# Optimization experiments

Measured on AMD Instinct MI355X. Metric: run time of the kernel, lower is better.

## Reference

```python
import jax, jax.numpy as jnp
import numpy as np

HIDDEN = 1024
HEADS = 16
HEAD_DIM = HIDDEN // HEADS
MAX_SEQ = 2048
BATCH = 2
SEQ = 2048


def setup_inputs() -> dict:
    key = jax.random.key(0)
    ks = jax.random.split(key, 6)
    x = jax.random.normal(ks[0], (BATCH, SEQ, HIDDEN), dtype=jnp.float32)
    # torch Linear params expressed as [in, out] weight + bias
    W1 = jax.random.normal(ks[1], (HIDDEN, 4 * HIDDEN), dtype=jnp.float32) * (HIDDEN ** -0.5)
    b1 = jnp.zeros((4 * HIDDEN,), dtype=jnp.float32)
    W2 = jax.random.normal(ks[2], (HIDDEN, HIDDEN), dtype=jnp.float32) * (HIDDEN ** -0.5)
    b2 = jnp.zeros((HIDDEN,), dtype=jnp.float32)
    rel_table = jax.random.normal(ks[3], (2 * MAX_SEQ - 1, HEADS), dtype=jnp.float32) * 0.02
    # causal mask [B, S, S]; True = keep
    attn_mask = jnp.broadcast_to(jnp.tril(jnp.ones((SEQ, SEQ), dtype=bool)), (BATCH, SEQ, SEQ))
    return {"x": x, "W1": W1, "b1": b1, "W2": W2, "b2": b2,
            "rel_table": rel_table, "attn_mask": attn_mask}


def reference(x, W1, b1, W2, b2, rel_table, attn_mask):
    B, S, H = x.shape
    # fused projection + SiLU, then chunk into U, Q, K, V
    activated = jax.nn.silu(jnp.einsum('bsh,hf->bsf', x, W1) + b1)
    U, Qp, Kp, Vp = jnp.split(activated, 4, axis=-1)
    # [B, nH, S, hd]
    def heads(t):
        return t.reshape(B, S, HEADS, HEAD_DIM).transpose(0, 2, 1, 3)
    Q, K, V = heads(Qp), heads(Kp), heads(Vp)
    scale = HEAD_DIM ** -0.5
    scores = jnp.einsum('bnqd,bnkd->bnqk', Q, K) * scale
    # relative position bias gather: idx[i,j] = i - j + MAX_SEQ - 1
    pos = jnp.arange(S)
    rel_idx = pos[:, None] - pos[None, :] + (MAX_SEQ - 1)  # [S, S]
    rel_bias = rel_table[rel_idx].transpose(2, 0, 1)[None]  # [1, nH, S, S]
    scores = scores + rel_bias
    attn = jax.nn.silu(scores)
    attn = jnp.where(attn_mask[:, None, :, :], attn, 0.0)
    out = jnp.einsum('bnqk,bnkd->bnqd', attn, V)
    out = out.transpose(0, 2, 1, 3).reshape(B, S, H)
    gated = out * U
    return jnp.einsum('bsh,hf->bsf', gated, W2) + b2
```

## Files before the change

kernel.cpp:

```cpp
#include <hip/hip_runtime.h>
#include <hip/hip_bf16.h>
#include <math.h>

#define HIDDEN   1024
#define HEADS    16
#define HEAD_DIM 64
#define SEQ      2048
#define BATCH    2
#define FDIM     4096
#define MTOT     4096
#define MAXSEQ   2048

typedef __bf16 bf16x8 __attribute__((ext_vector_type(8)));
typedef float  f32x4  __attribute__((ext_vector_type(4)));
typedef unsigned short u16;

__device__ __forceinline__ float silu_fast(float v) {
    return v * __builtin_amdgcn_rcpf(1.f + __expf(-v));
}

__device__ __forceinline__ u16 f2bf(float f) {
    union { float f; unsigned u; } v; v.f = f;
    unsigned r = v.u + 0x7FFFu + ((v.u >> 16) & 1u);
    return (u16)(r >> 16);
}
__device__ __forceinline__ float bf2f(u16 b) {
    union { unsigned u; float f; } v; v.u = ((unsigned)b) << 16;
    return v.f;
}
__device__ __forceinline__ unsigned pk2(float a, float b) {
    union { __hip_bfloat162 h; unsigned u; } z;
    z.h = __float22bfloat162_rn(make_float2(a, b));
    return z.u;
}

__device__ __forceinline__ void gload16(const void* g, void* l) {
    __builtin_amdgcn_global_load_lds(
        (const __attribute__((address_space(1))) void*)g,
        (__attribute__((address_space(3))) void*)l, 16, 0, 0);
}

__global__ __launch_bounds__(256) void prep_kernel(
    const float* __restrict__ X, const float* __restrict__ W1,
    const float* __restrict__ W2,
    u16* __restrict__ Xb, u16* __restrict__ W1t, u16* __restrict__ W2t,
    unsigned* __restrict__ ticket)
{
    __shared__ u16 T[64][72];
    const int tid = threadIdx.x;
    const int bid = blockIdx.x;

    if (bid == 0 && tid == 0) *ticket = 0u;

    if (bid < 2048) {
        int idx = (bid * 256 + tid) * 8;
        float4 a = *(const float4*)&X[idx];
        float4 b = *(const float4*)&X[idx + 4];
        uint4 pk = make_uint4(pk2(a.x, a.y), pk2(a.z, a.w),
                              pk2(b.x, b.y), pk2(b.z, b.w));
        *(uint4*)&Xb[idx] = pk;
        return;
    }

    const float* W; u16* Wt; int rows, cols, r0, c0;
    if (bid < 3072) {
        int t = bid - 2048;
        W = W1; Wt = W1t; rows = HIDDEN; cols = FDIM;
        c0 = (t & 63) * 64; r0 = (t >> 6) * 64;
    } else {
        int t = bid - 3072;
        W = W2; Wt = W2t; rows = HIDDEN; cols = HIDDEN;
        c0 = (t & 15) * 64; r0 = (t >> 4) * 64;
    }
#pragma unroll
    for (int l = 0; l < 4; ++l) {
        int idx = tid + l * 256;
        int row = idx >> 4;
        int c4  = (idx & 15) * 4;
        float4 v = *(const float4*)&W[(size_t)(r0 + row) * cols + c0 + c4];
        T[c4 + 0][row] = f2bf(v.x);
        T[c4 + 1][row] = f2bf(v.y);
        T[c4 + 2][row] = f2bf(v.z);
        T[c4 + 3][row] = f2bf(v.w);
    }
    __syncthreads();
#pragma unroll
    for (int l = 0; l < 2; ++l) {
        int idx = tid + l * 256;
        int row = idx >> 3;
        int cb  = (idx & 7) * 8;
        *(float4*)&Wt[(size_t)(c0 + row) * rows + r0 + cb] = *(float4*)&T[row][cb];
    }
}

#define GEMM_CORE(A_PTR, BT_PTR, KDIM, BM_, BN_, WMW, WNW)                     \
    enum { MTI = (BM_) / (WMW) / 16, NTI = (BN_) / (WNW) / 16,                 \
           ACH = (BM_) / 8, BCH = (BN_) / 8 };                                 \
    __shared__ __align__(16) u16 As[(BM_) * 64];                               \
    __shared__ __align__(16) u16 Bs[(BN_) * 64];                               \
    const int tid  = threadIdx.x;                                              \
    const int lane = tid & 63;                                                 \
    const int w    = tid >> 6;                                                 \
    const int wm   = w % (WMW), wn = w / (WMW);                                \
    const int l16  = lane & 15, quad = lane >> 4;                              \
    const int m0   = blockIdx.y * (BM_);                                       \
    const int n0   = blockIdx.x * (BN_);                                       \
    const int srow = lane >> 3;                                                \
    const int scol = (((lane & 7) ^ srow)) * 8;     \
    const int xr   = l16 & 7;                           \
    f32x4 acc[MTI][NTI];                                                       \
    _Pragma("unroll")                                                          \
    for (int mt = 0; mt < MTI; ++mt)                                           \
        _Pragma("unroll")                                                      \
        for (int nt = 0; nt < NTI; ++nt)                                       \
            acc[mt][nt] = (f32x4){0.f, 0.f, 0.f, 0.f};                         \
    for (int k0 = 0; k0 < (KDIM); k0 += 64) {                                  \
        __syncthreads();                                                       \
        _Pragma("unroll")                                                      \
        for (int ci = w; ci < ACH; ci += 4) {                                  \
            unsigned off = __builtin_amdgcn_readfirstlane(ci * 1024);          \
            gload16(&(A_PTR)[(size_t)(m0 + ci * 8 + srow) * (KDIM) + k0 + scol],\
                    (char*)As + off);                                          \
        }                                                                      \
        _Pragma("unroll")                                                      \
        for (int ci = w; ci < BCH; ci += 4) {                                  \
            unsigned off = __builtin_amdgcn_readfirstlane(ci * 1024);          \
            gload16(&(BT_PTR)[(size_t)(n0 + ci * 8 + srow) * (KDIM) + k0 + scol],\
                    (char*)Bs + off);                                          \
        }                                                                      \
        __syncthreads();                                                       \
        _Pragma("unroll")                                                      \
        for (int kc = 0; kc < 2; ++kc) {                                       \
            bf16x8 af[MTI], bfr[NTI];                                          \
            const int gsw = ((kc * 4 + quad) ^ xr) * 8;                        \
            _Pragma("unroll")                                                  \
            for (int t = 0; t < MTI; ++t)                                      \
                af[t]  = *(const bf16x8*)&As[(wm * (BM_ / WMW) + t * 16 + l16) \
                                             * 64 + gsw];                      \
            _Pragma("unroll")                                                  \
            for (int t = 0; t < NTI; ++t)                                      \
                bfr[t] = *(const bf16x8*)&Bs[(wn * (BN_ / WNW) + t * 16 + l16) \
                                             * 64 + gsw];                      \
            _Pragma("unroll")                                                  \
            for (int mt = 0; mt < MTI; ++mt)                                   \
                _Pragma("unroll")                                              \
                for (int nt = 0; nt < NTI; ++nt)                               \
                    acc[mt][nt] = __builtin_amdgcn_mfma_f32_16x16x32_bf16(     \
                        bfr[nt], af[mt], acc[mt][nt], 0, 0, 0);                \
        }                                                                      \
    }

__global__ __launch_bounds__(256, 1) void gemm1_mfma_kernel(
    const u16* __restrict__ A, const u16* __restrict__ Bt,
    const float* __restrict__ b1,
    u16* __restrict__ Ub, u16* __restrict__ Qh,
    u16* __restrict__ Kh, u16* __restrict__ Vh)
{
    GEMM_CORE(A, Bt, HIDDEN, 256, 128, 2, 2)

    const int chunk = n0 >> 10;
    u16* dstbase = (chunk == 0) ? Ub : (chunk == 1) ? Qh : (chunk == 2) ? Kh : Vh;
    const float postscale = (chunk == 1) ? 0.125f : 1.0f;

    float4 bias4[NTI]; int nloc[NTI];
#pragma unroll
    for (int nt = 0; nt < NTI; ++nt) {
        int nb = n0 + wn * 64 + nt * 16 + quad * 4;
        bias4[nt] = *(const float4*)&b1[nb];
        nloc[nt] = nb & 1023;
    }
#pragma unroll
    for (int mt = 0; mt < MTI; ++mt) {
        int m  = m0 + wm * 128 + mt * 16 + l16;
        int bb = m >> 11, s = m & 2047;
#pragma unroll
        for (int nt = 0; nt < NTI; ++nt) {
            float v0 = silu_fast(acc[mt][nt][0] + bias4[nt].x) * postscale;
            float v1 = silu_fast(acc[mt][nt][1] + bias4[nt].y) * postscale;
            float v2 = silu_fast(acc[mt][nt][2] + bias4[nt].z) * postscale;
            float v3 = silu_fast(acc[mt][nt][3] + bias4[nt].w) * postscale;
            uint2 pk = make_uint2(pk2(v0, v1), pk2(v2, v3));
            size_t o;
            if (chunk == 0) {
                o = (size_t)m * 1024 + nloc[nt];
            } else {
                int h = nloc[nt] >> 6, d = nloc[nt] & 63;
                o = (size_t)(((bb * HEADS + h) * SEQ) + s) * HEAD_DIM + d;
            }
            *(uint2*)&dstbase[o] = pk;
        }
    }
}

__global__ __launch_bounds__(256) void gemm2_mfma_kernel(
    const u16* __restrict__ A, const u16* __restrict__ Bt,
    const float* __restrict__ b2, float* __restrict__ Out)
{
    GEMM_CORE(A, Bt, HIDDEN, 64, 128, 1, 4)

    float4 bias4[NTI]; int nb[NTI];
#pragma unroll
    for (int nt = 0; nt < NTI; ++nt) {
        nb[nt] = n0 + wn * 32 + nt * 16 + quad * 4;
        bias4[nt] = *(const float4*)&b2[nb[nt]];
    }
#pragma unroll
    for (int mt = 0; mt < MTI; ++mt) {
        int m = m0 + mt * 16 + l16;
#pragma unroll
        for (int nt = 0; nt < NTI; ++nt) {
            float4 vv;
            vv.x = acc[mt][nt][0] + bias4[nt].x;
            vv.y = acc[mt][nt][1] + bias4[nt].y;
            vv.z = acc[mt][nt][2] + bias4[nt].z;
            vv.w = acc[mt][nt][3] + bias4[nt].w;
            *(float4*)&Out[(size_t)m * 1024 + nb[nt]] = vv;
        }
    }
}

__global__ __launch_bounds__(256, 3) void attn_mfma_kernel(
    const u16* __restrict__ Qh, const u16* __restrict__ Kh,
    const u16* __restrict__ Vh, const float* __restrict__ rel,
    const u16* __restrict__ Ub, u16* __restrict__ G,
    unsigned* __restrict__ ticket)
{
    __shared__ __align__(16) u16 Ks[128][72];
    __shared__ __align__(16) u16 Vt[64][136];
    __shared__ __align__(16) u16 Ps[2][64][64];
    __shared__ float rel_sh[192];
    __shared__ unsigned sh_t;

    const int tid  = threadIdx.x;
    const int lane = tid & 63;
    const int w    = tid >> 6;
    const int quad = lane >> 4;
    const int l16  = lane & 15;
    const int ws   = w & 1;
    const int pp   = w >> 1;
    const int qbase = ws * 32;
    const int xk   = l16 & 7;

    const int k_r = tid >> 3,       k_c = (tid & 7) * 8;
    const int v_k = (tid & 31) * 2, v_d = (tid >> 5) * 8;

    for (;;) {
        if (tid == 0) sh_t = atomicAdd(ticket, 1u);
        __syncthreads();
        const unsigned t = sh_t;
        if (t >= 1024u) return;

        const int qt = 31 - (int)(t >> 5);
        const int bh = (int)(t & 31u);
        const int h  = bh & 15;
        const int bb = bh >> 4;
        const int q0 = qt * 64;

        const u16* Kg = Kh + (size_t)((bb * HEADS + h) * SEQ) * HEAD_DIM;
        const u16* Vg = Vh + (size_t)((bb * HEADS + h) * SEQ) * HEAD_DIM;
        const u16* Qg = Qh + (size_t)((bb * HEADS + h) * SEQ + q0) * HEAD_DIM;

        bf16x8 qa[2][2];
#pragma unroll
        for (int sub = 0; sub < 2; ++sub) {
            const int qr = qbase + sub * 16 + l16;
            qa[sub][0] = *(const bf16x8*)&Qg[qr * HEAD_DIM + quad * 8];
            qa[sub][1] = *(const bf16x8*)&Qg[qr * HEAD_DIM + 32 + quad * 8];
        }

        float4 kA0 = *(const float4*)&Kg[(size_t)k_r * 64 + k_c];
        float4 kA1 = *(const float4*)&Kg[(size_t)(k_r + 32) * 64 + k_c];
        float4 vA0 = *(const float4*)&Vg[(size_t)v_k * 64 + v_d];
        float4 vA1 = *(const float4*)&Vg[(size_t)(v_k + 1) * 64 + v_d];
        float4 kB0, kB1, vB0, vB1;
        if (qt >= 1) {
            kB0 = *(const float4*)&Kg[(size_t)(64 + k_r) * 64 + k_c];
            kB1 = *(const float4*)&Kg[(size_t)(64 + k_r + 32) * 64 + k_c];
            vB0 = *(const float4*)&Vg[(size_t)(64 + v_k) * 64 + v_d];
            vB1 = *(const float4*)&Vg[(size_t)(64 + v_k + 1) * 64 + v_d];
        }
        float relreg = 0.f;
        if (tid < 191) relreg = rel[(size_t)(q0 + 1920 + tid) * HEADS + h];

        f32x4 o[2][4];
#pragma unroll
        for (int sub = 0; sub < 2; ++sub)
#pragma unroll
            for (int dt = 0; dt < 4; ++dt) o[sub][dt] = (f32x4){0.f, 0.f, 0.f, 0.f};

        for (int ip = 0; 2 * ip <= qt; ++ip) {
            const int kp = ip * 128;
            const bool hasB = (2 * ip + 1 <= qt);

            *(float4*)&Ks[k_r][k_c]      = kA0;
            *(float4*)&Ks[k_r + 32][k_c] = kA1;
            {
                union { float4 f; u16 u[8]; } a0, a1;
                a0.f = vA0; a1.f = vA1;
#pragma unroll
                for (int i = 0; i < 8; ++i)
                    *(unsigned*)&Vt[v_d + i][v_k] =
                        (unsigned)a0.u[i] | ((unsigned)a1.u[i] << 16);
            }
            if (hasB) {
                *(float4*)&Ks[64 + k_r][k_c]      = kB0;
                *(float4*)&Ks[64 + k_r + 32][k_c] = kB1;
                union { float4 f; u16 u[8]; } a0, a1;
                a0.f = vB0; a1.f = vB1;
#pragma unroll
                for (int i = 0; i < 8; ++i)
                    *(unsigned*)&Vt[v_d + i][64 + v_k] =
                        (unsigned)a0.u[i] | ((unsigned)a1.u[i] << 16);
            }
            if (tid < 191) rel_sh[tid] = relreg;
            __syncthreads();

            {
                const int nk0 = 2 * ip + 2;
                if (nk0 <= qt) {
                    const int b0 = nk0 * 64;
                    kA0 = *(const float4*)&Kg[(size_t)(b0 + k_r) * 64 + k_c];
                    kA1 = *(const float4*)&Kg[(size_t)(b0 + k_r + 32) * 64 + k_c];
                    vA0 = *(const float4*)&Vg[(size_t)(b0 + v_k) * 64 + v_d];
                    vA1 = *(const float4*)&Vg[(size_t)(b0 + v_k + 1) * 64 + v_d];
                    if (tid < 191)
                        relreg = rel[(size_t)(q0 - kp - 128 + 1920 + tid) * HEADS + h];
                    if (nk0 + 1 <= qt) {
                        const int b1 = b0 + 64;
                        kB0 = *(const float4*)&Kg[(size_t)(b1 + k_r) * 64 + k_c];
                        kB1 = *(const float4*)&Kg[(size_t)(b1 + k_r + 32) * 64 + k_c];
                        vB0 = *(const float4*)&Vg[(size_t)(b1 + v_k) * 64 + v_d];
                        vB1 = *(const float4*)&Vg[(size_t)(b1 + v_k + 1) * 64 + v_d];
                    }
                }
            }

            const int myc = 2 * ip + pp;
            if (myc <= qt) {
                const int ko      = pp * 64;
                const int relofs  = pp ? 63 : 127;
                const bool diag   = (myc == qt);
                const int qrelb   = q0 - kp - ko;

#pragma unroll
                for (int ct = 0; ct < 4; ++ct) {
                    bf16x8 ka0 = *(const bf16x8*)&Ks[ko + ct * 16 + l16][quad * 8];
                    bf16x8 ka1 = *(const bf16x8*)&Ks[ko + ct * 16 + l16][32 + quad * 8];
#pragma unroll
                    for (int sub = 0; sub < 2; ++sub) {
                        f32x4 sc = {0.f, 0.f, 0.f, 0.f};
                        sc = __builtin_amdgcn_mfma_f32_16x16x32_bf16(ka0, qa[sub][0], sc, 0, 0, 0);
                        sc = __builtin_amdgcn_mfma_f32_16x16x32_bf16(ka1, qa[sub][1], sc, 0, 0, 0);
                        const int qrow = qbase + sub * 16 + l16;
                        const int ib   = qrow - ct * 16 - quad * 4 + relofs;
                        float p4[4];
                        if (diag) {
#pragma unroll
                            for (int r = 0; r < 4; ++r) {
                                float s = sc[r] + rel_sh[ib - r];
                                int kloc = ct * 16 + quad * 4 + r;
                                p4[r] = (qrelb + qrow - kloc >= 0) ? silu_fast(s) : 0.f;
                            }
                        } else {
#pragma unroll
                            for (int r = 0; r < 4; ++r) {
                                float s = sc[r] + rel_sh[ib - r];
                                p4[r] = silu_fast(s);
                            }
                        }
                        const int col = (((2 * ct + (quad >> 1)) ^ xk) << 3) + (quad & 1) * 4;
                        *(uint2*)&Ps[pp][qrow][col] =
                            make_uint2(pk2(p4[0], p4[1]), pk2(p4[2], p4[3]));
                    }
                }

                bf16x8 pa0[2], pa1[2];
#pragma unroll
                for (int sub = 0; sub < 2; ++sub) {
                    const int qrow = qbase + sub * 16 + l16;
                    pa0[sub] = *(const bf16x8*)&Ps[pp][qrow][(quad ^ xk) * 8];
                    pa1[sub] = *(const bf16x8*)&Ps[pp][qrow][((4 + quad) ^ xk) * 8];
                }
#pragma unroll
                for (int dt = 0; dt < 4; ++dt) {
                    bf16x8 vb0 = *(const bf16x8*)&Vt[dt * 16 + l16][ko + quad * 8];
                    bf16x8 vb1 = *(const bf16x8*)&Vt[dt * 16 + l16][ko + 32 + quad * 8];
#pragma unroll
                    for (int sub = 0; sub < 2; ++sub) {
                        o[sub][dt] = __builtin_amdgcn_mfma_f32_16x16x32_bf16(pa0[sub], vb0, o[sub][dt], 0, 0, 0);
                        o[sub][dt] = __builtin_amdgcn_mfma_f32_16x16x32_bf16(pa1[sub], vb1, o[sub][dt], 0, 0, 0);
                    }
                }
            }
            __syncthreads();
        }

        float* Ored = (float*)&Ks[0][0];
        if (pp == 1) {
#pragma unroll
            for (int sub = 0; sub < 2; ++sub)
#pragma unroll
                for (int dt = 0; dt < 4; ++dt)
                    *(f32x4*)&Ored[((ws << 3) + (sub << 2) + dt) * 256 + lane * 4] =
                        o[sub][dt];
        }
        __syncthreads();
        if (pp == 0) {
#pragma unroll
            for (int sub = 0; sub < 2; ++sub)
#pragma unroll
                for (int dt = 0; dt < 4; ++dt) {
                    f32x4 r4 = *(const f32x4*)&Ored[((ws << 3) + (sub << 2) + dt) * 256 + lane * 4];
                    o[sub][dt] += r4;
#pragma unroll
                    for (int r = 0; r < 4; ++r) {
                        int q = q0 + qbase + sub * 16 + quad * 4 + r;
                        size_t base = (size_t)(bb * SEQ + q) * HIDDEN +
                                      h * HEAD_DIM + dt * 16 + l16;
                        float u = bf2f(Ub[base]);
                        G[base] = f2bf(o[sub][dt][r] * u);
                    }
                }
        }
    }
}

extern "C" void kernel_launch(void* const* d_in, const int* in_sizes, int n_in,
                              void* d_out, int out_size, void* d_ws, size_t ws_size,
                              hipStream_t stream)
{
    const float* X   = (const float*)d_in[0];
    const float* W1  = (const float*)d_in[1];
    const float* b1  = (const float*)d_in[2];
    const float* W2  = (const float*)d_in[3];
    const float* b2  = (const float*)d_in[4];
    const float* rel = (const float*)d_in[5];
    float* out = (float*)d_out;

    const size_t MH = (size_t)MTOT * HIDDEN;
    u16* Ub   = (u16*)d_ws;
    u16* Qh   = Ub  + MH;
    u16* Kh   = Qh  + MH;
    u16* Vh   = Kh  + MH;
    u16* Gbuf = Vh  + MH;
    u16* Xb   = Gbuf + MH;
    u16* W1t  = Xb  + MH;
    u16* W2t  = W1t + MH;
    unsigned* ticket = (unsigned*)(W2t + (size_t)HIDDEN * HIDDEN);

    prep_kernel<<<3328, 256, 0, stream>>>(X, W1, W2, Xb, W1t, W2t, ticket);
    gemm1_mfma_kernel<<<dim3(FDIM / 128, MTOT / 256), 256, 0, stream>>>(
        Xb, W1t, b1, Ub, Qh, Kh, Vh);
    attn_mfma_kernel<<<dim3(768), 256, 0, stream>>>(
        Qh, Kh, Vh, rel, Ub, Gbuf, ticket);
    gemm2_mfma_kernel<<<dim3(HIDDEN / 128, MTOT / 64), 256, 0, stream>>>(
        Gbuf, W2t, b2, out);
}
```

Before: 246.5 us.

## Transpose attention probabilities in registers via permlane swaps instead of LDS

Drops the shared-memory staging buffer for the SiLU probability tile. The S accumulator layout is rearranged into the MFMA A-operand layout with permlane32/permlane16 swap instructions. This removes LDS writes and reads from the inner loop and frees LDS, which lets the launch bounds rise to 4 blocks per CU and the persistent grid grow to 896 blocks. It relies on the permlane lane mapping matching the old swizzled layout exactly, and the higher occupancy target may tighten the register budget.

```diff
diff --git a/kernel.cpp b/kernel.cpp
--- a/kernel.cpp
+++ b/kernel.cpp
@@ -219,7 +219,7 @@
     }
 }
 
-__global__ __launch_bounds__(256, 3) void attn_mfma_kernel(
+__global__ __launch_bounds__(256, 4) void attn_mfma_kernel(
     const u16* __restrict__ Qh, const u16* __restrict__ Kh,
     const u16* __restrict__ Vh, const float* __restrict__ rel,
     const u16* __restrict__ Ub, u16* __restrict__ G,
@@ -227,7 +227,6 @@
 {
     __shared__ __align__(16) u16 Ks[128][72];
     __shared__ __align__(16) u16 Vt[64][136];
-    __shared__ __align__(16) u16 Ps[2][64][64];
     __shared__ float rel_sh[192];
     __shared__ unsigned sh_t;
 
@@ -239,7 +238,6 @@
     const int ws   = w & 1;
     const int pp   = w >> 1;
     const int qbase = ws * 32;
-    const int xk   = l16 & 7;
 
     const int k_r = tid >> 3,       k_c = (tid & 7) * 8;
     const int v_k = (tid & 31) * 2, v_d = (tid >> 5) * 8;
@@ -342,6 +340,7 @@
                 const bool diag   = (myc == qt);
                 const int qrelb   = q0 - kp - ko;
 
+                unsigned dw[2][4][2];
 #pragma unroll
                 for (int ct = 0; ct < 4; ++ct) {
                     bf16x8 ka0 = *(const bf16x8*)&Ks[ko + ct * 16 + l16][quad * 8];
@@ -368,27 +367,40 @@
                                 p4[r] = silu_fast(s);
                             }
                         }
-                        const int col = (((2 * ct + (quad >> 1)) ^ xk) << 3) + (quad & 1) * 4;
-                        *(uint2*)&Ps[pp][qrow][col] =
-                            make_uint2(pk2(p4[0], p4[1]), pk2(p4[2], p4[3]));
+                        dw[sub][ct][0] = pk2(p4[0], p4[1]);
+                        dw[sub][ct][1] = pk2(p4[2], p4[3]);
                     }
                 }
 
-                bf16x8 pa0[2], pa1[2];
+                union bfu { unsigned u[4]; bf16x8 v; };
+                bfu pa0[2], pa1[2];
 #pragma unroll
                 for (int sub = 0; sub < 2; ++sub) {
-                    const int qrow = qbase + sub * 16 + l16;
-                    pa0[sub] = *(const bf16x8*)&Ps[pp][qrow][(quad ^ xk) * 8];
-                    pa1[sub] = *(const bf16x8*)&Ps[pp][qrow][((4 + quad) ^ xk) * 8];
+#pragma unroll
+                    for (int s = 0; s < 2; ++s) {
+                        auto a = __builtin_amdgcn_permlane32_swap(
+                            dw[sub][0][s], dw[sub][1][s], false, false);
+                        auto x = __builtin_amdgcn_permlane16_swap(
+                            a[0], a[1], false, false);
+                        pa0[sub].u[s]     = x[0];
+                        pa0[sub].u[2 + s] = x[1];
+                        auto c = __builtin_amdgcn_permlane32_swap(
+                            dw[sub][2][s], dw[sub][3][s], false, false);
+                        auto y = __builtin_amdgcn_permlane16_swap(
+                            c[0], c[1], false, false);
+                        pa1[sub].u[s]     = y[0];
+                        pa1[sub].u[2 + s] = y[1];
+                    }
                 }
+
 #pragma unroll
                 for (int dt = 0; dt < 4; ++dt) {
                     bf16x8 vb0 = *(const bf16x8*)&Vt[dt * 16 + l16][ko + quad * 8];
                     bf16x8 vb1 = *(const bf16x8*)&Vt[dt * 16 + l16][ko + 32 + quad * 8];
 #pragma unroll
                     for (int sub = 0; sub < 2; ++sub) {
-                        o[sub][dt] = __builtin_amdgcn_mfma_f32_16x16x32_bf16(pa0[sub], vb0, o[sub][dt], 0, 0, 0);
-                        o[sub][dt] = __builtin_amdgcn_mfma_f32_16x16x32_bf16(pa1[sub], vb1, o[sub][dt], 0, 0, 0);
+                        o[sub][dt] = __builtin_amdgcn_mfma_f32_16x16x32_bf16(pa0[sub].v, vb0, o[sub][dt], 0, 0, 0);
+                        o[sub][dt] = __builtin_amdgcn_mfma_f32_16x16x32_bf16(pa1[sub].v, vb1, o[sub][dt], 0, 0, 0);
                     }
                 }
             }
@@ -451,7 +463,7 @@
     prep_kernel<<<3328, 256, 0, stream>>>(X, W1, W2, Xb, W1t, W2t, ticket);
     gemm1_mfma_kernel<<<dim3(FDIM / 128, MTOT / 256), 256, 0, stream>>>(
         Xb, W1t, b1, Ub, Qh, Kh, Vh);
-    attn_mfma_kernel<<<dim3(768), 256, 0, stream>>>(
+    attn_mfma_kernel<<<dim3(896), 256, 0, stream>>>(
         Qh, Kh, Vh, rel, Ub, Gbuf, ticket);
     gemm2_mfma_kernel<<<dim3(HIDDEN / 128, MTOT / 64), 256, 0, stream>>>(
         Gbuf, W2t, b2, out);
```

Result: slower. 331.4 us (+34.5%).
